# Kernel tuning notes

Measured on AMD Instinct MI355X. Metric: run time of the kernel, lower is better.

The kernel has to match this reference:

```python
import jax, jax.numpy as jnp
import numpy as np

EPS = 1e-6
N, CHANNEL, M, K, D = 4096, 1024, 8, 2048, 128


def setup_inputs() -> dict:
    key = jax.random.key(0)
    ks = jax.random.split(key, 7)
    std = float(np.sqrt(2.0 / (5.0 * CHANNEL / M)))  # matches nn.init.normal_ std in __init__
    return {
        "x": jax.random.normal(ks[0], (N, CHANNEL), dtype=jnp.float32),
        "codebook0": jax.random.normal(ks[1], (M, K, D), dtype=jnp.float32) * std,
        "codebook1": jax.random.normal(ks[2], (M, K, D), dtype=jnp.float32) * std,
        "temperature0": jnp.ones((M, 1), dtype=jnp.float32),
        "temperature1": jnp.ones((M, 1), dtype=jnp.float32),
        "u0": jax.random.uniform(ks[3], (N, M, K), dtype=jnp.float32),
        "u1": jax.random.uniform(ks[4], (N, M, K), dtype=jnp.float32),
    }


def _distance(z, codebook):
    # z: (n, m, d), codebook: (m, k, d) -> (n, m, k) squared euclidean
    x2 = jnp.sum(z * z, axis=-1, keepdims=True)          # (n, m, 1)
    c2 = jnp.sum(codebook * codebook, axis=-1)           # (m, k)
    inter = jnp.einsum('nmd,mkd->nmk', z, codebook)      # (n, m, k)
    return x2 + c2 - 2.0 * inter


def _level(x, codebook, temperature, u):
    # One _quantizerEncoder level with Identity heads.
    n = x.shape[0]
    m, k, d = codebook.shape
    z = x.reshape(n, m, d)
    scale = jnp.asarray(np.sqrt(k), dtype=x.dtype)
    # logit = -distance / sqrt(k) * LowerBound(temperature, Eps)
    logit = (-_distance(z, codebook) / scale) * jnp.maximum(temperature, EPS)
    # gumbel-softmax, tau=1.0, hard=True (permutationRate == 0 -> no permutation)
    uc = jnp.clip(u, EPS, 1.0 - EPS)
    gumbel = -jnp.log(-jnp.log(uc))
    y = jax.nn.softmax(logit + gumbel, axis=-1)          # (n, m, k)
    hard_idx = jnp.argmax(y, axis=-1)                    # (n, m)
    y_hard = jax.nn.one_hot(hard_idx, k, dtype=y.dtype)
    sample = y_hard + y - jax.lax.stop_gradient(y)       # straight-through
    # _multiCodebookDeQuantization.forward
    deq = jnp.einsum('nmk,mkd->nmd', sample, codebook).reshape(n, m * d)
    return sample, deq, logit


def reference(x, codebook0, codebook1, temperature0, temperature1, u0, u1):
    # Encoder pass (Identity latentStageEncoder/quantizationHead/latentHead)
    _, deq0, _ = _level(x, codebook0, temperature0, u0)
    x1 = x - deq0                                        # residual to next level
    _, deq1, _ = _level(x1, codebook1, temperature1, u1)
    # Decoder pass, reversed (Identity dequantizationHead/sideHead/restoreHead):
    # formerLevel = decode(level1); xHat = deq0 + sideHead(formerLevel)
    former = deq1
    xHat = deq0 + former
    return xHat
```

## Files before the change

### kernel.cpp

```cpp
#include <hip/hip_runtime.h>
#include <math.h>


namespace {
constexpr int Mm = 8, Kk = 2048, Dd = 128;
constexpr int MK = Mm * Kk;
constexpr double SQRTK = 45.254833995939045;

__device__ __forceinline__ double wsum_d(double v) {
#pragma unroll
  for (int o = 32; o > 0; o >>= 1) v += __shfl_xor(v, o);
  return v;
}
__device__ __forceinline__ float wsum_f(float v) {
#pragma unroll
  for (int o = 32; o > 0; o >>= 1) v += __shfl_xor(v, o);
  return v;
}
__device__ __forceinline__ float wmax_f(float v) {
#pragma unroll
  for (int o = 32; o > 0; o >>= 1) v = fmaxf(v, __shfl_xor(v, o));
  return v;
}

__device__ __forceinline__ double gumbel_d(float u) {
  double uc = fmin(fmax((double)u, 1e-6), 1.0 - 1e-6);
  return -log(-log(uc));
}

__device__ __forceinline__ float gumbel_lb_f(float u) {
  float uc = fminf(fmaxf(u, 1e-6f), 1.0f - 1e-6f);
  float e = 1.0f - uc;
  float t;
  if (e > 0.04f) {
    t = -__logf(uc);
  } else {
    t = e * (1.0f + e * (0.5f + e * (0.3333334f + e * 0.25f)));
  }
  t *= 1.000004f;
  return -__logf(t) - 2e-5f;
}

__global__ __launch_bounds__(256) void prep1(
    const float* __restrict__ cb0, const float* __restrict__ cb1,
    double* __restrict__ c2d0, double* __restrict__ c2d1) {
  int wid = threadIdx.x >> 6, lane = threadIdx.x & 63;
  int row = blockIdx.x * 4 + wid;
  int lvl = row >= MK;
  int r = row & (MK - 1);
  const float* cb = lvl ? cb1 : cb0;
  float2 c = ((const float2*)(cb + (size_t)r * Dd))[lane];
  double s = wsum_d((double)c.x * (double)c.x + (double)c.y * (double)c.y);
  if (lane == 0) { if (lvl) c2d1[r] = s; else c2d0[r] = s; }
}

__global__ __launch_bounds__(256) void prep2(
    const double* __restrict__ c2d0, const double* __restrict__ c2d1,
    const float* __restrict__ t0, const float* __restrict__ t1,
    float2* __restrict__ Rtab) {
  int b = blockIdx.x;
  int lvl = b >> 3, m = b & 7;
  const double* c2 = (lvl ? c2d1 : c2d0) + m * Kk;
  int tid = threadIdx.x;
  double mx = -1e300, mn = 1e300;
  for (int i = tid; i < Kk; i += 256) { double v = c2[i]; mx = fmax(mx, v); mn = fmin(mn, v); }
#pragma unroll
  for (int o = 32; o > 0; o >>= 1) {
    mx = fmax(mx, __shfl_xor(mx, o));
    mn = fmin(mn, __shfl_xor(mn, o));
  }
  __shared__ double smx[4], smn[4];
  int wid = tid >> 6, lane = tid & 63;
  if (lane == 0) { smx[wid] = mx; smn[wid] = mn; }
  __syncthreads();
  if (tid == 0) {
    mx = fmax(fmax(smx[0], smx[1]), fmax(smx[2], smx[3]));
    mn = fmin(fmin(smn[0], smn[1]), fmin(smn[2], smn[3]));
    double w = (double)fmaxf(lvl ? t1[m] : t0[m], 1e-6f) / SQRTK;
    float2 r;
    r.x = (float)(w * (mx - mn) * 1.0001);
    r.y = (float)(4.0 * w * sqrt(mx) * 1.0001);
    Rtab[b] = r;
  }
}

__device__ __forceinline__ int do_level(
    float zx, float zy, int lane, float um, const float4* r,
    const float* __restrict__ urow,
    const float* __restrict__ cbm,
    const double* __restrict__ c2m,
    float2 rr, double wd, float2* bc_out) {
  float zn = sqrtf(wsum_f(zx * zx + zy * zy));
  float thr = gumbel_lb_f(um) - (rr.x + rr.y * zn) - 0.05f;
  float uthr = __expf(-__expf(-thr) * 1.000004f) * (1.0f - 4e-6f);
  unsigned mask32 = 0;
#pragma unroll
  for (int j = 0; j < 8; ++j) {
    mask32 |= (r[j].x >= uthr ? 1u : 0u) << (j * 4 + 0);
    mask32 |= (r[j].y >= uthr ? 1u : 0u) << (j * 4 + 1);
    mask32 |= (r[j].z >= uthr ? 1u : 0u) << (j * 4 + 2);
    mask32 |= (r[j].w >= uthr ? 1u : 0u) << (j * 4 + 3);
  }
  double bestS = -1e300;
  int bestK = 0;
  float2 bc = make_float2(0.f, 0.f);
  for (;;) {
    bool has = (mask32 != 0);
    unsigned long long actv = __ballot(has);
    if (!actv) break;
    int kc = 0;
    double g = 0.0;
    if (has) {
      int t = __builtin_ffs((int)mask32) - 1;
      mask32 &= mask32 - 1;
      kc = ((t >> 2) << 8) + (lane << 2) + (t & 3);
      g = gumbel_d(urow[kc]);
    }
    while (actv) {
      int l = (int)__ffsll(actv) - 1;
      actv &= actv - 1;
      int kcl = __shfl(kc, l);
      double gl = __shfl(g, l);
      float2 c = ((const float2*)(cbm + (size_t)kcl * Dd))[lane];
      double dot = wsum_d((double)zx * (double)c.x + (double)zy * (double)c.y);
      double sc = (2.0 * dot - c2m[kcl]) * wd + gl;
      if (sc > bestS || (sc == bestS && kcl < bestK)) {
        bestS = sc; bestK = kcl; bc = c;
      }
    }
  }
  *bc_out = bc;
  return bestK;
}

__global__ __launch_bounds__(256) void fused_kernel(
    const float* __restrict__ x,
    const float* __restrict__ cb0, const float* __restrict__ cb1,
    const float* __restrict__ t0, const float* __restrict__ t1,
    const float* __restrict__ u0, const float* __restrict__ u1,
    const double* __restrict__ c2d0, const double* __restrict__ c2d1,
    const float2* __restrict__ Rtab,
    float* __restrict__ out) {
  const int wid = threadIdx.x >> 6, lane = threadIdx.x & 63;
  const int p = blockIdx.x * 4 + wid;
  const int m = p >> 12;
  const int n = p & 4095;

  const float* u0row = u0 + ((size_t)n * Mm + m) * Kk;
  const float* u1row = u1 + ((size_t)n * Mm + m) * Kk;
  const float4* a4 = (const float4*)u0row;
  const float4* b4 = (const float4*)u1row;

  float4 r0[8], r1[8];
#pragma unroll
  for (int j = 0; j < 8; ++j) { r0[j] = a4[j * 64 + lane]; r1[j] = b4[j * 64 + lane]; }

  float2 z = ((const float2*)(x + (size_t)n * 1024 + m * Dd))[lane];
  double wd0 = (double)fmaxf(t0[m], 1e-6f) / SQRTK;
  double wd1 = (double)fmaxf(t1[m], 1e-6f) / SQRTK;

  float um0 = 0.f, um1 = 0.f;
#pragma unroll
  for (int j = 0; j < 8; ++j) {
    um0 = fmaxf(um0, fmaxf(fmaxf(r0[j].x, r0[j].y), fmaxf(r0[j].z, r0[j].w)));
    um1 = fmaxf(um1, fmaxf(fmaxf(r1[j].x, r1[j].y), fmaxf(r1[j].z, r1[j].w)));
  }
  um0 = wmax_f(um0);
  um1 = wmax_f(um1);

  const float* cb0m = cb0 + (size_t)m * Kk * Dd;
  const float* cb1m = cb1 + (size_t)m * Kk * Dd;

  float2 c0, c1;
  (void)do_level(z.x, z.y, lane, um0, r0, u0row, cb0m, c2d0 + m * Kk,
                 Rtab[m], wd0, &c0);
  (void)do_level(z.x - c0.x, z.y - c0.y, lane, um1, r1, u1row, cb1m,
                 c2d1 + m * Kk, Rtab[8 + m], wd1, &c1);

  ((float2*)(out + (size_t)n * 1024 + m * Dd))[lane] =
      make_float2(c0.x + c1.x, c0.y + c1.y);
}
}

extern "C" void kernel_launch(void* const* d_in, const int* in_sizes, int n_in,
                              void* d_out, int out_size, void* d_ws, size_t ws_size,
                              hipStream_t stream) {
  const float* x   = (const float*)d_in[0];
  const float* cb0 = (const float*)d_in[1];
  const float* cb1 = (const float*)d_in[2];
  const float* t0  = (const float*)d_in[3];
  const float* t1  = (const float*)d_in[4];
  const float* u0  = (const float*)d_in[5];
  const float* u1  = (const float*)d_in[6];
  float* out = (float*)d_out;

  char* ws = (char*)d_ws;
  double* c2d0 = (double*)ws;
  double* c2d1 = c2d0 + MK;
  float2* Rtab = (float2*)(c2d1 + MK);

  prep1<<<8192, 256, 0, stream>>>(cb0, cb1, c2d0, c2d1);
  prep2<<<16, 256, 0, stream>>>(c2d0, c2d1, t0, t1, Rtab);
  fused_kernel<<<8192, 256, 0, stream>>>(x, cb0, cb1, t0, t1, u0, u1,
                                         c2d0, c2d1, Rtab, out);
}
```

Measured before the change: 562.6 us.

## Compute both level candidate masks upfront and software-pipeline codebook row fetches

New measurement: 730.3 us. 1.3x slower.

```diff
diff --git a/kernel.cpp b/kernel.cpp
--- a/kernel.cpp
+++ b/kernel.cpp
@@ -10,16 +10,6 @@
 __device__ __forceinline__ double wsum_d(double v) {
 #pragma unroll
   for (int o = 32; o > 0; o >>= 1) v += __shfl_xor(v, o);
-  return v;
-}
-__device__ __forceinline__ float wsum_f(float v) {
-#pragma unroll
-  for (int o = 32; o > 0; o >>= 1) v += __shfl_xor(v, o);
-  return v;
-}
-__device__ __forceinline__ float wmax_f(float v) {
-#pragma unroll
-  for (int o = 32; o > 0; o >>= 1) v = fmaxf(v, __shfl_xor(v, o));
   return v;
 }
 
@@ -57,7 +47,7 @@
 __global__ __launch_bounds__(256) void prep2(
     const double* __restrict__ c2d0, const double* __restrict__ c2d1,
     const float* __restrict__ t0, const float* __restrict__ t1,
-    float2* __restrict__ Rtab) {
+    float4* __restrict__ Rtab) {
   int b = blockIdx.x;
   int lvl = b >> 3, m = b & 7;
   const double* c2 = (lvl ? c2d1 : c2d0) + m * Kk;
@@ -77,60 +67,13 @@
     mx = fmax(fmax(smx[0], smx[1]), fmax(smx[2], smx[3]));
     mn = fmin(fmin(smn[0], smn[1]), fmin(smn[2], smn[3]));
     double w = (double)fmaxf(lvl ? t1[m] : t0[m], 1e-6f) / SQRTK;
-    float2 r;
+    float4 r;
     r.x = (float)(w * (mx - mn) * 1.0001);
     r.y = (float)(4.0 * w * sqrt(mx) * 1.0001);
+    r.z = (float)(sqrt(mx) * 1.0001);
+    r.w = 0.f;
     Rtab[b] = r;
   }
-}
-
-__device__ __forceinline__ int do_level(
-    float zx, float zy, int lane, float um, const float4* r,
-    const float* __restrict__ urow,
-    const float* __restrict__ cbm,
-    const double* __restrict__ c2m,
-    float2 rr, double wd, float2* bc_out) {
-  float zn = sqrtf(wsum_f(zx * zx + zy * zy));
-  float thr = gumbel_lb_f(um) - (rr.x + rr.y * zn) - 0.05f;
-  float uthr = __expf(-__expf(-thr) * 1.000004f) * (1.0f - 4e-6f);
-  unsigned mask32 = 0;
-#pragma unroll
-  for (int j = 0; j < 8; ++j) {
-    mask32 |= (r[j].x >= uthr ? 1u : 0u) << (j * 4 + 0);
-    mask32 |= (r[j].y >= uthr ? 1u : 0u) << (j * 4 + 1);
-    mask32 |= (r[j].z >= uthr ? 1u : 0u) << (j * 4 + 2);
-    mask32 |= (r[j].w >= uthr ? 1u : 0u) << (j * 4 + 3);
-  }
-  double bestS = -1e300;
-  int bestK = 0;
-  float2 bc = make_float2(0.f, 0.f);
-  for (;;) {
-    bool has = (mask32 != 0);
-    unsigned long long actv = __ballot(has);
-    if (!actv) break;
-    int kc = 0;
-    double g = 0.0;
-    if (has) {
-      int t = __builtin_ffs((int)mask32) - 1;
-      mask32 &= mask32 - 1;
-      kc = ((t >> 2) << 8) + (lane << 2) + (t & 3);
-      g = gumbel_d(urow[kc]);
-    }
-    while (actv) {
-      int l = (int)__ffsll(actv) - 1;
-      actv &= actv - 1;
-      int kcl = __shfl(kc, l);
-      double gl = __shfl(g, l);
-      float2 c = ((const float2*)(cbm + (size_t)kcl * Dd))[lane];
-      double dot = wsum_d((double)zx * (double)c.x + (double)zy * (double)c.y);
-      double sc = (2.0 * dot - c2m[kcl]) * wd + gl;
-      if (sc > bestS || (sc == bestS && kcl < bestK)) {
-        bestS = sc; bestK = kcl; bc = c;
-      }
-    }
-  }
-  *bc_out = bc;
-  return bestK;
 }
 
 __global__ __launch_bounds__(256) void fused_kernel(
@@ -139,7 +82,7 @@
     const float* __restrict__ t0, const float* __restrict__ t1,
     const float* __restrict__ u0, const float* __restrict__ u1,
     const double* __restrict__ c2d0, const double* __restrict__ c2d1,
-    const float2* __restrict__ Rtab,
+    const float4* __restrict__ Rtab,
     float* __restrict__ out) {
   const int wid = threadIdx.x >> 6, lane = threadIdx.x & 63;
   const int p = blockIdx.x * 4 + wid;
@@ -151,34 +94,144 @@
   const float4* a4 = (const float4*)u0row;
   const float4* b4 = (const float4*)u1row;
 
-  float4 r0[8], r1[8];
-#pragma unroll
-  for (int j = 0; j < 8; ++j) { r0[j] = a4[j * 64 + lane]; r1[j] = b4[j * 64 + lane]; }
-
+  float um0 = 0.f, um1 = 0.f;
+#pragma unroll
+  for (int j = 0; j < 8; ++j) {
+    float4 a = a4[j * 64 + lane];
+    float4 b = b4[j * 64 + lane];
+    um0 = fmaxf(um0, fmaxf(fmaxf(a.x, a.y), fmaxf(a.z, a.w)));
+    um1 = fmaxf(um1, fmaxf(fmaxf(b.x, b.y), fmaxf(b.z, b.w)));
+  }
   float2 z = ((const float2*)(x + (size_t)n * 1024 + m * Dd))[lane];
-  double wd0 = (double)fmaxf(t0[m], 1e-6f) / SQRTK;
-  double wd1 = (double)fmaxf(t1[m], 1e-6f) / SQRTK;
-
-  float um0 = 0.f, um1 = 0.f;
+  float ss = z.x * z.x + z.y * z.y;
+#pragma unroll
+  for (int o = 32; o > 0; o >>= 1) {
+    um0 = fmaxf(um0, __shfl_xor(um0, o));
+    um1 = fmaxf(um1, __shfl_xor(um1, o));
+    ss += __shfl_xor(ss, o);
+  }
+  float zn = sqrtf(ss);
+
+  const float4 R0 = Rtab[m], R1 = Rtab[8 + m];
+  float thr0 = gumbel_lb_f(um0) - (R0.x + R0.y * zn) - 0.05f;
+  float uthr0 = __expf(-__expf(-thr0) * 1.000004f) * (1.0f - 4e-6f);
+  float zn1ub = zn + R0.z;
+  float thr1 = gumbel_lb_f(um1) - (R1.x + R1.y * zn1ub) - 0.05f;
+  float uthr1 = __expf(-__expf(-thr1) * 1.000004f) * (1.0f - 4e-6f);
+
+  unsigned mask0 = 0, mask1 = 0;
 #pragma unroll
   for (int j = 0; j < 8; ++j) {
-    um0 = fmaxf(um0, fmaxf(fmaxf(r0[j].x, r0[j].y), fmaxf(r0[j].z, r0[j].w)));
-    um1 = fmaxf(um1, fmaxf(fmaxf(r1[j].x, r1[j].y), fmaxf(r1[j].z, r1[j].w)));
-  }
-  um0 = wmax_f(um0);
-  um1 = wmax_f(um1);
-
+    float4 a = a4[j * 64 + lane];
+    float4 b = b4[j * 64 + lane];
+    mask0 |= (a.x >= uthr0 ? 1u : 0u) << (j * 4 + 0);
+    mask0 |= (a.y >= uthr0 ? 1u : 0u) << (j * 4 + 1);
+    mask0 |= (a.z >= uthr0 ? 1u : 0u) << (j * 4 + 2);
+    mask0 |= (a.w >= uthr0 ? 1u : 0u) << (j * 4 + 3);
+    mask1 |= (b.x >= uthr1 ? 1u : 0u) << (j * 4 + 0);
+    mask1 |= (b.y >= uthr1 ? 1u : 0u) << (j * 4 + 1);
+    mask1 |= (b.z >= uthr1 ? 1u : 0u) << (j * 4 + 2);
+    mask1 |= (b.w >= uthr1 ? 1u : 0u) << (j * 4 + 3);
+  }
+
+  const double wd0 = (double)fmaxf(t0[m], 1e-6f) / SQRTK;
+  const double wd1 = (double)fmaxf(t1[m], 1e-6f) / SQRTK;
   const float* cb0m = cb0 + (size_t)m * Kk * Dd;
   const float* cb1m = cb1 + (size_t)m * Kk * Dd;
-
-  float2 c0, c1;
-  (void)do_level(z.x, z.y, lane, um0, r0, u0row, cb0m, c2d0 + m * Kk,
-                 Rtab[m], wd0, &c0);
-  (void)do_level(z.x - c0.x, z.y - c0.y, lane, um1, r1, u1row, cb1m,
-                 c2d1 + m * Kk, Rtab[8 + m], wd1, &c1);
+  const double* c2m0 = c2d0 + m * Kk;
+  const double* c2m1 = c2d1 + m * Kk;
+
+  int hk0 = 0, hk1 = 0;
+  double hg0 = 0.0, hg1 = 0.0;
+  if (mask0) {
+    int t = __builtin_ffs((int)mask0) - 1;
+    hk0 = ((t >> 2) << 8) + (lane << 2) + (t & 3);
+    hg0 = gumbel_d(u0row[hk0]);
+  }
+  if (mask1) {
+    int t = __builtin_ffs((int)mask1) - 1;
+    hk1 = ((t >> 2) << 8) + (lane << 2) + (t & 3);
+    hg1 = gumbel_d(u1row[hk1]);
+  }
+
+  auto pop0 = [&](int& okc, double& og) -> bool {
+    unsigned long long actv = __ballot(mask0 != 0);
+    if (!actv) return false;
+    int l = (int)__ffsll(actv) - 1;
+    okc = __shfl(hk0, l);
+    og = __shfl(hg0, l);
+    if (lane == l) {
+      mask0 &= mask0 - 1;
+      if (mask0) {
+        int t = __builtin_ffs((int)mask0) - 1;
+        hk0 = ((t >> 2) << 8) + (lane << 2) + (t & 3);
+        hg0 = gumbel_d(u0row[hk0]);
+      }
+    }
+    return true;
+  };
+  auto pop1 = [&](int& okc, double& og) -> bool {
+    unsigned long long actv = __ballot(mask1 != 0);
+    if (!actv) return false;
+    int l = (int)__ffsll(actv) - 1;
+    okc = __shfl(hk1, l);
+    og = __shfl(hg1, l);
+    if (lane == l) {
+      mask1 &= mask1 - 1;
+      if (mask1) {
+        int t = __builtin_ffs((int)mask1) - 1;
+        hk1 = ((t >> 2) << 8) + (lane << 2) + (t & 3);
+        hg1 = gumbel_d(u1row[hk1]);
+      }
+    }
+    return true;
+  };
+  auto fill = [&](int& okc, double& og, float2& oc, double& oc2) -> int {
+    int kcl; double gl;
+    if (pop0(kcl, gl)) {
+      oc = ((const float2*)(cb0m + (size_t)kcl * Dd))[lane];
+      oc2 = c2m0[kcl];
+      okc = kcl; og = gl;
+      return 0;
+    }
+    if (pop1(kcl, gl)) {
+      oc = ((const float2*)(cb1m + (size_t)kcl * Dd))[lane];
+      oc2 = c2m1[kcl];
+      okc = kcl; og = gl;
+      return 1;
+    }
+    return -1;
+  };
+
+  int Akc = 0, Bkc = 0;
+  double Ag = 0.0, Bg = 0.0, Ac2 = 0.0, Bc2 = 0.0;
+  float2 Ac = make_float2(0.f, 0.f), Bc = make_float2(0.f, 0.f);
+  int Alvl = fill(Akc, Ag, Ac, Ac2);
+  int Blvl = (Alvl >= 0) ? fill(Bkc, Bg, Bc, Bc2) : -1;
+
+  double best0 = -1e300, best1 = -1e300;
+  int bk0 = 0, bk1 = 0;
+  float2 bc0 = make_float2(0.f, 0.f), bc1 = make_float2(0.f, 0.f);
+  float z1x = 0.f, z1y = 0.f;
+  bool z1rdy = false;
+
+  while (Alvl >= 0) {
+    if (Alvl == 0) {
+      double dot = wsum_d((double)z.x * (double)Ac.x + (double)z.y * (double)Ac.y);
+      double sc = (2.0 * dot - Ac2) * wd0 + Ag;
+      if (sc > best0 || (sc == best0 && Akc < bk0)) { best0 = sc; bk0 = Akc; bc0 = Ac; }
+    } else {
+      if (!z1rdy) { z1x = z.x - bc0.x; z1y = z.y - bc0.y; z1rdy = true; }
+      double dot = wsum_d((double)z1x * (double)Ac.x + (double)z1y * (double)Ac.y);
+      double sc = (2.0 * dot - Ac2) * wd1 + Ag;
+      if (sc > best1 || (sc == best1 && Akc < bk1)) { best1 = sc; bk1 = Akc; bc1 = Ac; }
+    }
+    Alvl = Blvl; Akc = Bkc; Ag = Bg; Ac = Bc; Ac2 = Bc2;
+    Blvl = (Alvl >= 0) ? fill(Bkc, Bg, Bc, Bc2) : -1;
+  }
 
   ((float2*)(out + (size_t)n * 1024 + m * Dd))[lane] =
-      make_float2(c0.x + c1.x, c0.y + c1.y);
+      make_float2(bc0.x + bc1.x, bc0.y + bc1.y);
 }
 }
 
@@ -197,7 +250,7 @@
   char* ws = (char*)d_ws;
   double* c2d0 = (double*)ws;
   double* c2d1 = c2d0 + MK;
-  float2* Rtab = (float2*)(c2d1 + MK);
+  float4* Rtab = (float4*)(c2d1 + MK);
 
   prep1<<<8192, 256, 0, stream>>>(cb0, cb1, c2d0, c2d1);
   prep2<<<16, 256, 0, stream>>>(c2d0, c2d1, t0, t1, Rtab);
```
